# Kernel optimization log

Measured on AMD Instinct MI355X. Metric: run time of the kernel, lower is better.

## Reference

```python
import jax, jax.numpy as jnp
import numpy as np

THRESH = 0.85

def setup_inputs() -> dict:
    key = jax.random.key(0)
    k1, k2 = jax.random.split(key)
    bs, d, r, c = 4, 16, 64, 64
    n = r * c
    seg = jax.random.normal(k1, (bs, d, r, c), dtype=jnp.float32)
    W = jax.random.uniform(k2, (bs, n, n), dtype=jnp.float32)
    return {"seg": seg, "W": W}

def reference(seg, W):
    bs, d, r, c = seg.shape
    # threshold affinity: keep values > 0.85
    Wt = jnp.where(W > THRESH, W, jnp.zeros((), W.dtype))
    # row-normalize: D = diag(1/rowsum(Wt)) @ Wt  (broadcast division)
    D = Wt / Wt.sum(axis=-1, keepdims=True)          # [bs, n, n]
    seg_flat = seg.reshape(bs, d, r * c)             # [bs, d, n]
    # seg_flat @ D^T : out[b,d,m] = sum_n seg[b,d,n] * D[b,m,n]
    out = jnp.einsum('bdn,bmn->bdm', seg_flat, D)
    return out.reshape(bs, d, r, c)
```

## Files before the change

### kernel.cpp

```cpp
#include <hip/hip_runtime.h>
#include <stdint.h>


typedef float v4f __attribute__((ext_vector_type(4)));

#define N_DIM 4096
#define D_DIM 16
#define THRESH 0.85f
#define RPW 4
#define CHUNK 256
#define NCHUNK (N_DIM / CHUNK)

__global__ __launch_bounds__(256) void regu_kernel(
    const float* __restrict__ seg,
    const float* __restrict__ W,
    float* __restrict__ out)
{
    __shared__ float stile[2][D_DIM * CHUNK];

    const int lane = threadIdx.x & 63;
    const int wv   = threadIdx.x >> 6;
    const int row0 = blockIdx.x * 16 + wv * RPW;
    const int b  = row0 >> 12;
    const int m0 = row0 & (N_DIM - 1);

    const float* Wp   = W   + ((size_t)b * N_DIM + m0) * N_DIM + lane * 4;
    const float* segb = seg + (size_t)b * D_DIM * N_DIM;

    float acc[RPW * D_DIM];
    float rowsum[RPW] = {0.f, 0.f, 0.f, 0.f};
#pragma unroll
    for (int i = 0; i < RPW * D_DIM; ++i) acc[i] = 0.f;

#define STAGE(c, sb)                                                          \
    do {                                                                      \
        _Pragma("unroll")                                                     \
        for (int j = 0; j < 4; ++j) {                                         \
            const int d_ = wv * 4 + j;                                        \
            const float* g_ = segb + (size_t)d_ * N_DIM + (c) * CHUNK + lane * 4; \
            __builtin_amdgcn_global_load_lds(                                 \
                (const __attribute__((address_space(1))) uint32_t*)g_,        \
                (__attribute__((address_space(3))) uint32_t*)&stile[sb][d_ * CHUNK], \
                16, 0, 0);                                                    \
        }                                                                     \
    } while (0)

    v4f wA[RPW], wB[RPW];

    STAGE(0, 0);
#pragma unroll
    for (int r = 0; r < RPW; ++r)
        wA[r] = __builtin_nontemporal_load((const v4f*)(Wp + (size_t)r * N_DIM));
    __syncthreads();

    auto compute = [&](const v4f* w_in, int sb) {
        v4f w[RPW];
#pragma unroll
        for (int r = 0; r < RPW; ++r) {
            v4f v = w_in[r];
            v.x = (v.x > THRESH) ? v.x : 0.f;
            v.y = (v.y > THRESH) ? v.y : 0.f;
            v.z = (v.z > THRESH) ? v.z : 0.f;
            v.w = (v.w > THRESH) ? v.w : 0.f;
            w[r] = v;
            rowsum[r] += (v.x + v.y) + (v.z + v.w);
        }
#pragma unroll
        for (int d = 0; d < D_DIM; ++d) {
            const v4f s = *(const v4f*)&stile[sb][d * CHUNK + lane * 4];
#pragma unroll
            for (int r = 0; r < RPW; ++r) {
                acc[r * D_DIM + d] += w[r].x * s.x;
                acc[r * D_DIM + d] += w[r].y * s.y;
                acc[r * D_DIM + d] += w[r].z * s.z;
                acc[r * D_DIM + d] += w[r].w * s.w;
            }
        }
    };

    for (int c = 0; c < NCHUNK; c += 2) {
        STAGE(c + 1, 1);
        {
            const float* p = Wp + (size_t)(c + 1) * CHUNK;
#pragma unroll
            for (int r = 0; r < RPW; ++r)
                wB[r] = __builtin_nontemporal_load((const v4f*)(p + (size_t)r * N_DIM));
        }
        compute(wA, 0);
        __syncthreads();

        if (c + 2 < NCHUNK) {
            STAGE(c + 2, 0);
            const float* p = Wp + (size_t)(c + 2) * CHUNK;
#pragma unroll
            for (int r = 0; r < RPW; ++r)
                wA[r] = __builtin_nontemporal_load((const v4f*)(p + (size_t)r * N_DIM));
        }
        compute(wB, 1);
        __syncthreads();
    }

#pragma unroll
    for (int k = 0; k < 6; ++k) {
        const int S = 32 >> k;
        const bool up = (lane >> k) & 1;
#pragma unroll
        for (int j = 0; j < S; ++j) {
            const float mine = up ? acc[j + S] : acc[j];
            const float send = up ? acc[j] : acc[j + S];
            acc[j] = mine + __shfl_xor(send, 1 << k, 64);
        }
    }

#pragma unroll
    for (int r = 0; r < RPW; ++r) {
        float s = rowsum[r];
#pragma unroll
        for (int off = 1; off < 64; off <<= 1) s += __shfl_xor(s, off, 64);
        rowsum[r] = s;
    }

    const int j = __brev((unsigned)lane) >> 26;
    const int r = j >> 4;
    const int d = j & 15;
    const float inv = 1.0f / (r < 2 ? (r == 0 ? rowsum[0] : rowsum[1])
                                    : (r == 2 ? rowsum[2] : rowsum[3]));
    out[((size_t)b * D_DIM + d) * N_DIM + (m0 + r)] = acc[0] * inv;
}

extern "C" void kernel_launch(void* const* d_in, const int* in_sizes, int n_in,
                              void* d_out, int out_size, void* d_ws, size_t ws_size,
                              hipStream_t stream) {
    const float* seg = (const float*)d_in[0];
    const float* W   = (const float*)d_in[1];
    float* out = (float*)d_out;

    regu_kernel<<<1024, 256, 0, stream>>>(seg, W, out);
}
```

Baseline: 355.2 us.

## Deepen seg/W prefetch pipeline to four LDS buffers with vmcnt-based waits

Replaces the two-buffer double-buffered loop with a four-slot LDS ring and two register sets for W. Each phase waits with a manual s_waitcnt vmcnt(8) plus a raw barrier instead of __syncthreads, so loads for chunk c+2 can stay in flight while chunk c is computed. The aim is to keep more memory traffic outstanding on this bandwidth-bound W stream. It doubles LDS use and relies on exact counting of outstanding vector-memory ops, which is fragile if the compiler reorders or splits loads.

```diff
diff --git a/kernel.cpp b/kernel.cpp
--- a/kernel.cpp
+++ b/kernel.cpp
@@ -16,7 +16,7 @@
     const float* __restrict__ W,
     float* __restrict__ out)
 {
-    __shared__ float stile[2][D_DIM * CHUNK];
+    __shared__ float stile[4][D_DIM * CHUNK];
 
     const int lane = threadIdx.x & 63;
     const int wv   = threadIdx.x >> 6;
@@ -37,7 +37,7 @@
         _Pragma("unroll")                                                     \
         for (int j = 0; j < 4; ++j) {                                         \
             const int d_ = wv * 4 + j;                                        \
-            const float* g_ = segb + (size_t)d_ * N_DIM + (c) * CHUNK + lane * 4; \
+            const float* g_ = segb + (size_t)d_ * N_DIM + (size_t)(c) * CHUNK + lane * 4; \
             __builtin_amdgcn_global_load_lds(                                 \
                 (const __attribute__((address_space(1))) uint32_t*)g_,        \
                 (__attribute__((address_space(3))) uint32_t*)&stile[sb][d_ * CHUNK], \
@@ -45,15 +45,18 @@
         }                                                                     \
     } while (0)
 
-    v4f wA[RPW], wB[RPW];
+#define LOADW(dst, c)                                                         \
+    do {                                                                      \
+        const float* p_ = Wp + (size_t)(c) * CHUNK;                           \
+        _Pragma("unroll")                                                     \
+        for (int r = 0; r < RPW; ++r)                                         \
+            dst[r] = __builtin_nontemporal_load(                              \
+                (const v4f*)(p_ + (size_t)r * N_DIM));                        \
+    } while (0)
 
-    STAGE(0, 0);
-#pragma unroll
-    for (int r = 0; r < RPW; ++r)
-        wA[r] = __builtin_nontemporal_load((const v4f*)(Wp + (size_t)r * N_DIM));
-    __syncthreads();
+    v4f wR0[RPW], wR1[RPW];
 
-    auto compute = [&](const v4f* w_in, int sb) {
+    auto compute = [&](const v4f (&w_in)[RPW], const int sb) {
         v4f w[RPW];
 #pragma unroll
         for (int r = 0; r < RPW; ++r) {
@@ -78,27 +81,33 @@
         }
     };
 
-    for (int c = 0; c < NCHUNK; c += 2) {
-        STAGE(c + 1, 1);
-        {
-            const float* p = Wp + (size_t)(c + 1) * CHUNK;
-#pragma unroll
-            for (int r = 0; r < RPW; ++r)
-                wB[r] = __builtin_nontemporal_load((const v4f*)(p + (size_t)r * N_DIM));
-        }
-        compute(wA, 0);
-        __syncthreads();
+    STAGE(0, 0); LOADW(wR0, 0);
+    asm volatile("" ::: "memory");
+    STAGE(1, 1); LOADW(wR1, 1);
 
-        if (c + 2 < NCHUNK) {
-            STAGE(c + 2, 0);
-            const float* p = Wp + (size_t)(c + 2) * CHUNK;
-#pragma unroll
-            for (int r = 0; r < RPW; ++r)
-                wA[r] = __builtin_nontemporal_load((const v4f*)(p + (size_t)r * N_DIM));
-        }
-        compute(wB, 1);
-        __syncthreads();
+#define PHASE(cexp, sb, wname, sb2)                                  \
+    do {                                                             \
+        const int c_ = (cexp);                                       \
+        if (c_ < NCHUNK - 1)                                         \
+            asm volatile("s_waitcnt vmcnt(8)" ::: "memory");         \
+        else                                                         \
+            asm volatile("s_waitcnt vmcnt(0)" ::: "memory");         \
+        __builtin_amdgcn_s_barrier();                                \
+        if (c_ + 2 < NCHUNK) STAGE(c_ + 2, sb2);                     \
+        compute(wname, sb);                                          \
+        if (c_ + 2 < NCHUNK) LOADW(wname, c_ + 2);                   \
+    } while (0)
+
+    for (int cc = 0; cc < NCHUNK; cc += 4) {
+        PHASE(cc + 0, 0, wR0, 2);
+        PHASE(cc + 1, 1, wR1, 3);
+        PHASE(cc + 2, 2, wR0, 0);
+        PHASE(cc + 3, 3, wR1, 1);
     }
+
+#undef PHASE
+#undef LOADW
+#undef STAGE
 
 #pragma unroll
     for (int k = 0; k < 6; ++k) {
```

Result: slower. 376.4 us (+6.0%).
